# Performance work log

Measured on AMD Instinct MI355X. Metric: run time of the kernel, lower is better.

The kernel has to match this reference:

```python
import jax, jax.numpy as jnp
import numpy as np

N_HEAD = 16
D_MODEL = 1024
D_K = D_MODEL // N_HEAD  # 64, also d_v
B, S = 8, 1024


def setup_inputs() -> dict:
    key = jax.random.key(0)
    ks = jax.random.split(key, 7)
    sc = 1.0 / np.sqrt(D_MODEL)
    return {
        "q": jax.random.normal(ks[0], (B, S, D_MODEL), jnp.float32),
        "k": jax.random.normal(ks[1], (B, S, D_MODEL), jnp.float32),
        "v": jax.random.normal(ks[2], (B, S, D_MODEL), jnp.float32),
        "Wq": jax.random.normal(ks[3], (N_HEAD, D_MODEL, D_K), jnp.float32) * sc,
        "Wk": jax.random.normal(ks[4], (N_HEAD, D_MODEL, D_K), jnp.float32) * sc,
        "Wv": jax.random.normal(ks[5], (D_MODEL, D_K), jnp.float32) * sc,  # shared across heads
        "Wo": jax.random.normal(ks[6], (D_K, D_MODEL), jnp.float32) * (1.0 / np.sqrt(D_K)),
    }


def reference(q, k, v, Wq, Wk, Wv, Wo):
    # Faithful to original: qs, ks, vs are ALL projected from q (k, v args unused),
    # and Wv is shared across all heads. Dropout is identity (rate 0 / eval).
    qs = jnp.einsum('bsd,hdk->hbsk', q, Wq)          # [H,B,S,dk]
    kk = jnp.einsum('bsd,hdk->hbsk', q, Wk)          # [H,B,S,dk]
    vs = jnp.einsum('bsd,dk->bsk', q, Wv)            # [B,S,dv] shared
    scale = 1.0 / jnp.sqrt(jnp.asarray(D_K, jnp.float32))
    scores = jnp.einsum('hbik,hbjk->hbij', qs, kk) * scale  # [H,B,S,S]
    attn = jax.nn.softmax(scores, axis=-1)
    head = jnp.einsum('hbij,bjk->hbik', attn, vs)    # [H,B,S,dv]
    pooled = jnp.mean(head, axis=0)                  # mean over heads, not concat
    out = jnp.einsum('bsk,kd->bsd', pooled, Wo)      # [B,S,d_model]
    return (out, attn)
```

## Files before the change

kernel.cpp:

```cpp
#include <hip/hip_runtime.h>
#include <hip/hip_bf16.h>
#include <stdint.h>

#define NC 2112

typedef __attribute__((ext_vector_type(8))) short bf16x8;
typedef __attribute__((ext_vector_type(4))) float f32x4;

static __device__ __forceinline__ unsigned short f2bf(float f) {
  uint32_t u = __builtin_bit_cast(uint32_t, f);
  u += 0x7FFFu + ((u >> 16) & 1u);
  return (unsigned short)(u >> 16);
}
static __device__ __forceinline__ unsigned short f2bf_n(float f) {
  __hip_bfloat16 h = __float2bfloat16(f);
  return __builtin_bit_cast(unsigned short, h);
}
static __device__ __forceinline__ float bf2f(unsigned short u) {
  return __builtin_bit_cast(float, ((uint32_t)u) << 16);
}
static __device__ __forceinline__ void gload16(const unsigned short* g, unsigned short* l) {
  __builtin_amdgcn_global_load_lds((const __attribute__((address_space(1))) void*)g,
                                   (__attribute__((address_space(3))) void*)l, 16, 0, 0);
}

__global__ void k_convert_q(const float* __restrict__ q, unsigned short* __restrict__ qbf) {
  int i = blockIdx.x * blockDim.x + threadIdx.x;
  float4 v = ((const float4*)q)[i];
  ushort4 o;
  o.x = f2bf(v.x); o.y = f2bf(v.y); o.z = f2bf(v.z); o.w = f2bf(v.w);
  ((ushort4*)qbf)[i] = o;
}

__global__ void k_build_wcatT(const float* __restrict__ Wq, const float* __restrict__ Wk,
                              const float* __restrict__ Wv, unsigned short* __restrict__ wt) {
  int t = blockIdx.x * blockDim.x + threadIdx.x;
  int c = t >> 7;
  int k0 = (t & 127) << 3;
  unsigned short o[8];
#pragma unroll
  for (int i = 0; i < 8; ++i) {
    int k = k0 + i;
    float v;
    if (c < 1024)      v = Wq[((size_t)(c >> 6) * 1024 + k) * 64 + (c & 63)];
    else if (c < 2048) v = Wk[((size_t)((c - 1024) >> 6) * 1024 + k) * 64 + (c & 63)];
    else               v = Wv[(size_t)k * 64 + (c - 2048)];
    o[i] = f2bf(v);
  }
  *(ushort4*)&wt[(size_t)c * 1024 + k0]     = *(ushort4*)&o[0];
  *(ushort4*)&wt[(size_t)c * 1024 + k0 + 4] = *(ushort4*)&o[4];
}

__global__ __launch_bounds__(256) void k_gemm(const unsigned short* __restrict__ A,
                                              const unsigned short* __restrict__ Bt,
                                              unsigned short* __restrict__ C,
                                              unsigned short* __restrict__ vst) {
  __shared__ unsigned short As[128 * 32];
  __shared__ unsigned short Bs[128 * 32];
  const int L = blockIdx.x;
  const int wi = (L & 7) * 136 + (L >> 3);
  const int tn = wi % 17, tm = wi / 17;
  const int rowBase = tm * 128, colBase = tn * 128;
  const int t = threadIdx.x;
  const int wave = t >> 6, lane = t & 63;
  const int wm = wave >> 1, wn = wave & 1;
  const int l15 = lane & 15, l4 = lane >> 4;
  f32x4 acc[4][4] = {};
  for (int kt = 0; kt < 1024; kt += 32) {
#pragma unroll
    for (int i = 0; i < 2; ++i) {
      int e = (t + i * 256) * 8;
      int r = e >> 5, c = e & 31;
      gload16(&A[(size_t)(rowBase + r) * 1024 + kt + c], &As[e]);
      int rb = colBase + r; rb = rb < NC ? rb : (NC - 1);
      gload16(&Bt[(size_t)rb * 1024 + kt + c], &Bs[e]);
    }
    __syncthreads();
    bf16x8 af[4], bfr[4];
#pragma unroll
    for (int m = 0; m < 4; ++m) af[m] = *(const bf16x8*)&As[(wm * 64 + m * 16 + l15) * 32 + l4 * 8];
#pragma unroll
    for (int n = 0; n < 4; ++n) bfr[n] = *(const bf16x8*)&Bs[(wn * 64 + n * 16 + l15) * 32 + l4 * 8];
#pragma unroll
    for (int m = 0; m < 4; ++m)
#pragma unroll
      for (int n = 0; n < 4; ++n)
        acc[m][n] = __builtin_amdgcn_mfma_f32_16x16x32_bf16(af[m], bfr[n], acc[m][n], 0, 0, 0);
    __syncthreads();
  }
#pragma unroll
  for (int m = 0; m < 4; ++m)
#pragma unroll
    for (int n = 0; n < 4; ++n) {
      int col = colBase + wn * 64 + n * 16 + l15;
      int row0 = rowBase + wm * 64 + m * 16 + l4 * 4;
      if (col < 2048) {
#pragma unroll
        for (int i = 0; i < 4; ++i)
          C[(size_t)(row0 + i) * NC + col] = f2bf_n(acc[m][n][i]);
      } else if (col < NC) {
        int d = col - 2048;
#pragma unroll
        for (int i = 0; i < 4; ++i) {
          int rg = row0 + i;
          vst[((size_t)(rg >> 10) * 64 + d) * 1024 + (rg & 1023)] = f2bf_n(acc[m][n][i]);
        }
      }
    }
}

__global__ __launch_bounds__(512, 4) void k_attn(const unsigned short* __restrict__ G,
                                                 const unsigned short* __restrict__ vst,
                                                 float* __restrict__ attn,
                                                 float* __restrict__ head) {
  __shared__ unsigned short SP[32][1032];
  __shared__ float rs[32][8];
  const int L = blockIdx.x;
  const int wi = (L & 7) * 512 + (L >> 3);
  const int qt = wi & 31, b = (wi >> 5) & 7, h = wi >> 8;
  const int t = threadIdx.x, wave = t >> 6, lane = t & 63;
  const int l15 = lane & 15, l4 = lane >> 4;

  const unsigned short* Gb = G + (size_t)b * 1024 * NC;

  bf16x8 qf[2][2];
#pragma unroll
  for (int m = 0; m < 2; ++m)
#pragma unroll
    for (int ks = 0; ks < 2; ++ks)
      qf[m][ks] = *(const bf16x8*)&Gb[(size_t)(qt * 32 + m * 16 + l15) * NC + h * 64 + ks * 32 + l4 * 8];

  const float scale = 0.125f;
  float psum[2][4] = {};
#pragma unroll
  for (int half = 0; half < 2; ++half) {
    bf16x8 kf[4][2];
#pragma unroll
    for (int kt = 0; kt < 4; ++kt) {
      int k0 = wave * 128 + (half * 4 + kt) * 16;
#pragma unroll
      for (int ks = 0; ks < 2; ++ks)
        kf[kt][ks] = *(const bf16x8*)&Gb[(size_t)(k0 + l15) * NC + 1024 + h * 64 + ks * 32 + l4 * 8];
    }
#pragma unroll
    for (int kt = 0; kt < 4; ++kt) {
      int k0 = wave * 128 + (half * 4 + kt) * 16;
      f32x4 s0 = {}, s1 = {};
      __builtin_amdgcn_s_setprio(1);
      s0 = __builtin_amdgcn_mfma_f32_16x16x32_bf16(qf[0][0], kf[kt][0], s0, 0, 0, 0);
      s0 = __builtin_amdgcn_mfma_f32_16x16x32_bf16(qf[0][1], kf[kt][1], s0, 0, 0, 0);
      s1 = __builtin_amdgcn_mfma_f32_16x16x32_bf16(qf[1][0], kf[kt][0], s1, 0, 0, 0);
      s1 = __builtin_amdgcn_mfma_f32_16x16x32_bf16(qf[1][1], kf[kt][1], s1, 0, 0, 0);
      __builtin_amdgcn_s_setprio(0);
#pragma unroll
      for (int i = 0; i < 4; ++i) {
        unsigned short u0 = f2bf_n(__expf(s0[i] * scale));
        unsigned short u1 = f2bf_n(__expf(s1[i] * scale));
        SP[l4 * 4 + i][k0 + l15]      = u0;
        SP[16 + l4 * 4 + i][k0 + l15] = u1;
        psum[0][i] += bf2f(u0);
        psum[1][i] += bf2f(u1);
      }
    }
  }
#pragma unroll
  for (int off = 1; off < 16; off <<= 1)
#pragma unroll
    for (int m = 0; m < 2; ++m)
#pragma unroll
      for (int i = 0; i < 4; ++i)
        psum[m][i] += __shfl_xor(psum[m][i], off);
  if (l15 == 0) {
#pragma unroll
    for (int m = 0; m < 2; ++m)
#pragma unroll
      for (int i = 0; i < 4; ++i)
        rs[m * 16 + l4 * 4 + i][wave] = psum[m][i];
  }
  __syncthreads();

  const int wm = wave >> 2, wn = wave & 3;
  float winv[4], pinv[4];
#pragma unroll
  for (int rr = 0; rr < 4; ++rr) {
    int row = wave * 4 + rr;
    float4 a = *(const float4*)&rs[row][0];
    float4 c = *(const float4*)&rs[row][4];
    winv[rr] = 1.0f / (a.x + a.y + a.z + a.w + c.x + c.y + c.z + c.w);
  }
#pragma unroll
  for (int i = 0; i < 4; ++i) {
    int row = wm * 16 + l4 * 4 + i;
    float4 a = *(const float4*)&rs[row][0];
    float4 c = *(const float4*)&rs[row][4];
    pinv[i] = 1.0f / (a.x + a.y + a.z + a.w + c.x + c.y + c.z + c.w);
  }

  size_t attn_base = ((size_t)(h * 8 + b) * 1024 + (size_t)qt * 32) * 1024;
#pragma unroll
  for (int rr = 0; rr < 4; ++rr) {
    int row = wave * 4 + rr;
    float inv = winv[rr];
#pragma unroll
    for (int c = 0; c < 2; ++c) {
      uint4 u = *(const uint4*)&SP[row][c * 512 + lane * 8];
      f32x4 p0 = {bf2f((unsigned short)(u.x & 0xFFFF)) * inv,
                  bf2f((unsigned short)(u.x >> 16)) * inv,
                  bf2f((unsigned short)(u.y & 0xFFFF)) * inv,
                  bf2f((unsigned short)(u.y >> 16)) * inv};
      f32x4 p1 = {bf2f((unsigned short)(u.z & 0xFFFF)) * inv,
                  bf2f((unsigned short)(u.z >> 16)) * inv,
                  bf2f((unsigned short)(u.w & 0xFFFF)) * inv,
                  bf2f((unsigned short)(u.w >> 16)) * inv};
      float* ab = &attn[attn_base + (size_t)row * 1024 + c * 512 + lane * 8];
      __builtin_nontemporal_store(p0, (f32x4*)ab);
      __builtin_nontemporal_store(p1, (f32x4*)(ab + 4));
    }
  }

  const unsigned short* vb = vst + ((size_t)b * 64 + wn * 16 + l15) * 1024;
  const unsigned short* pr = &SP[wm * 16 + l15][0];
  f32x4 o0 = {}, o1 = {};
  __builtin_amdgcn_s_setprio(1);
#pragma unroll 8
  for (int jt = 0; jt < 32; jt += 2) {
    bf16x8 pa0 = *(const bf16x8*)&pr[jt * 32 + l4 * 8];
    bf16x8 bv0 = *(const bf16x8*)&vb[jt * 32 + l4 * 8];
    o0 = __builtin_amdgcn_mfma_f32_16x16x32_bf16(pa0, bv0, o0, 0, 0, 0);
    bf16x8 pa1 = *(const bf16x8*)&pr[(jt + 1) * 32 + l4 * 8];
    bf16x8 bv1 = *(const bf16x8*)&vb[(jt + 1) * 32 + l4 * 8];
    o1 = __builtin_amdgcn_mfma_f32_16x16x32_bf16(pa1, bv1, o1, 0, 0, 0);
  }
  __builtin_amdgcn_s_setprio(0);
  float* hb = head + (((size_t)(h * 8 + b) * 1024) + qt * 32 + wm * 16) * 64 + wn * 16;
#pragma unroll
  for (int i = 0; i < 4; ++i)
    hb[(size_t)(l4 * 4 + i) * 64 + l15] = (o0[i] + o1[i]) * pinv[i];
}

__global__ __launch_bounds__(256) void k_final(const float* __restrict__ head,
                                               const float* __restrict__ Wo,
                                               float* __restrict__ out) {
  __shared__ float Ps[32][68];
  __shared__ float Ws[64][132];
  const int rt = blockIdx.x;
  const int r0 = rt * 32;
  const int t = threadIdx.x;
#pragma unroll
  for (int j = 0; j < 2; ++j) {
    int e = t + j * 256;
    int r = e >> 4, k4 = (e & 15) * 4;
    float4 acc = {0.f, 0.f, 0.f, 0.f};
#pragma unroll
    for (int hh = 0; hh < 16; ++hh) {
      float4 v = *(const float4*)&head[((size_t)hh * 8192 + r0 + r) * 64 + k4];
      acc.x += v.x; acc.y += v.y; acc.z += v.z; acc.w += v.w;
    }
    const float s = 1.0f / 16.0f;
    Ps[r][k4] = acc.x * s; Ps[r][k4 + 1] = acc.y * s;
    Ps[r][k4 + 2] = acc.z * s; Ps[r][k4 + 3] = acc.w * s;
  }
  const int ty = t >> 4, tx = t & 15;
  for (int dt = 0; dt < 8; ++dt) {
    int d0 = dt * 128;
#pragma unroll
    for (int j = 0; j < 8; ++j) {
      int e = t + j * 256;
      int k = e >> 5, c4 = (e & 31) * 4;
      *(float4*)&Ws[k][c4] = *(const float4*)&Wo[(size_t)k * 1024 + d0 + c4];
    }
    __syncthreads();
    float acc[2][8] = {};
    for (int k = 0; k < 64; ++k) {
      float a0 = Ps[ty * 2][k], a1 = Ps[ty * 2 + 1][k];
      float4 b0 = *(const float4*)&Ws[k][tx * 8];
      float4 b1 = *(const float4*)&Ws[k][tx * 8 + 4];
      acc[0][0] += a0 * b0.x; acc[0][1] += a0 * b0.y; acc[0][2] += a0 * b0.z; acc[0][3] += a0 * b0.w;
      acc[0][4] += a0 * b1.x; acc[0][5] += a0 * b1.y; acc[0][6] += a0 * b1.z; acc[0][7] += a0 * b1.w;
      acc[1][0] += a1 * b0.x; acc[1][1] += a1 * b0.y; acc[1][2] += a1 * b0.z; acc[1][3] += a1 * b0.w;
      acc[1][4] += a1 * b1.x; acc[1][5] += a1 * b1.y; acc[1][6] += a1 * b1.z; acc[1][7] += a1 * b1.w;
    }
#pragma unroll
    for (int i = 0; i < 2; ++i) {
      float4 v0 = {acc[i][0], acc[i][1], acc[i][2], acc[i][3]};
      float4 v1 = {acc[i][4], acc[i][5], acc[i][6], acc[i][7]};
      size_t o = (size_t)(r0 + ty * 2 + i) * 1024 + d0 + tx * 8;
      *(float4*)&out[o]     = v0;
      *(float4*)&out[o + 4] = v1;
    }
    __syncthreads();
  }
}

extern "C" void kernel_launch(void* const* d_in, const int* in_sizes, int n_in,
                              void* d_out, int out_size, void* d_ws, size_t ws_size,
                              hipStream_t stream) {
  const float* q  = (const float*)d_in[0];
  const float* Wq = (const float*)d_in[3];
  const float* Wk = (const float*)d_in[4];
  const float* Wv = (const float*)d_in[5];
  const float* Wo = (const float*)d_in[6];

  char* ws = (char*)d_ws;
  unsigned short* qbf   = (unsigned short*)(ws + 0);
  unsigned short* wcatT = (unsigned short*)(ws + 16777216);
  unsigned short* G     = (unsigned short*)(ws + 21102592);
  unsigned short* vst   = (unsigned short*)(ws + 55705600);
  float*          head  = (float*)(ws + 56754176);

  float* out  = (float*)d_out;
  float* attn = out + (size_t)8 * 1024 * 1024;

  hipLaunchKernelGGL(k_convert_q,   dim3(8192), dim3(256), 0, stream, q, qbf);
  hipLaunchKernelGGL(k_build_wcatT, dim3(1056), dim3(256), 0, stream, Wq, Wk, Wv, wcatT);
  hipLaunchKernelGGL(k_gemm,        dim3(1088), dim3(256), 0, stream, qbf, wcatT, G, vst);
  hipLaunchKernelGGL(k_attn,        dim3(4096), dim3(512), 0, stream, G, vst, attn, head);
  hipLaunchKernelGGL(k_final,       dim3(256),  dim3(256), 0, stream, head, Wo, out);
}
```

Measured before the change: 355.7 us.

## Halve attention query tile to 16 rows and split PV over key halves

The attention kernel now handles 16 query rows per block instead of 32, which doubles the grid and halves shared memory for the probability tile. Launch bounds now request 8 blocks per CU instead of 4, to raise occupancy. The PV product is split across two key halves per wave group and reduced through shared memory with an extra barrier. In exchange, each K tile is reused by fewer query rows, so K loads per output roughly double, and the extra sync adds latency.

```diff
diff --git a/kernel.cpp b/kernel.cpp
--- a/kernel.cpp
+++ b/kernel.cpp
@@ -109,97 +109,86 @@
     }
 }
 
-__global__ __launch_bounds__(512, 4) void k_attn(const unsigned short* __restrict__ G,
+__global__ __launch_bounds__(512, 8) void k_attn(const unsigned short* __restrict__ G,
                                                  const unsigned short* __restrict__ vst,
                                                  float* __restrict__ attn,
                                                  float* __restrict__ head) {
-  __shared__ unsigned short SP[32][1032];
-  __shared__ float rs[32][8];
+  __shared__ unsigned short SP[16][1032];
+  __shared__ float rs[16][8];
+  __shared__ float red[4][16][17];
   const int L = blockIdx.x;
-  const int wi = (L & 7) * 512 + (L >> 3);
-  const int qt = wi & 31, b = (wi >> 5) & 7, h = wi >> 8;
+  const int wi = (L & 7) * 1024 + (L >> 3);
+  const int qt = wi & 63, b = (wi >> 6) & 7, h = wi >> 9;
   const int t = threadIdx.x, wave = t >> 6, lane = t & 63;
   const int l15 = lane & 15, l4 = lane >> 4;
+  const float scale = 0.125f;
 
   const unsigned short* Gb = G + (size_t)b * 1024 * NC;
 
-  bf16x8 qf[2][2];
-#pragma unroll
-  for (int m = 0; m < 2; ++m)
-#pragma unroll
-    for (int ks = 0; ks < 2; ++ks)
-      qf[m][ks] = *(const bf16x8*)&Gb[(size_t)(qt * 32 + m * 16 + l15) * NC + h * 64 + ks * 32 + l4 * 8];
-
-  const float scale = 0.125f;
-  float psum[2][4] = {};
-#pragma unroll
-  for (int half = 0; half < 2; ++half) {
-    bf16x8 kf[4][2];
-#pragma unroll
-    for (int kt = 0; kt < 4; ++kt) {
-      int k0 = wave * 128 + (half * 4 + kt) * 16;
+  bf16x8 qf[2];
+#pragma unroll
+  for (int ks = 0; ks < 2; ++ks)
+    qf[ks] = *(const bf16x8*)&Gb[(size_t)(qt * 16 + l15) * NC + h * 64 + ks * 32 + l4 * 8];
+
+  float psum[4] = {};
+#pragma unroll
+  for (int half = 0; half < 4; ++half) {
+    bf16x8 kf[2][2];
+#pragma unroll
+    for (int kt = 0; kt < 2; ++kt) {
+      int k0 = wave * 128 + (half * 2 + kt) * 16;
 #pragma unroll
       for (int ks = 0; ks < 2; ++ks)
         kf[kt][ks] = *(const bf16x8*)&Gb[(size_t)(k0 + l15) * NC + 1024 + h * 64 + ks * 32 + l4 * 8];
     }
 #pragma unroll
-    for (int kt = 0; kt < 4; ++kt) {
-      int k0 = wave * 128 + (half * 4 + kt) * 16;
-      f32x4 s0 = {}, s1 = {};
+    for (int kt = 0; kt < 2; ++kt) {
+      int k0 = wave * 128 + (half * 2 + kt) * 16;
+      f32x4 s = {};
       __builtin_amdgcn_s_setprio(1);
-      s0 = __builtin_amdgcn_mfma_f32_16x16x32_bf16(qf[0][0], kf[kt][0], s0, 0, 0, 0);
-      s0 = __builtin_amdgcn_mfma_f32_16x16x32_bf16(qf[0][1], kf[kt][1], s0, 0, 0, 0);
-      s1 = __builtin_amdgcn_mfma_f32_16x16x32_bf16(qf[1][0], kf[kt][0], s1, 0, 0, 0);
-      s1 = __builtin_amdgcn_mfma_f32_16x16x32_bf16(qf[1][1], kf[kt][1], s1, 0, 0, 0);
+      s = __builtin_amdgcn_mfma_f32_16x16x32_bf16(qf[0], kf[kt][0], s, 0, 0, 0);
+      s = __builtin_amdgcn_mfma_f32_16x16x32_bf16(qf[1], kf[kt][1], s, 0, 0, 0);
       __builtin_amdgcn_s_setprio(0);
 #pragma unroll
       for (int i = 0; i < 4; ++i) {
-        unsigned short u0 = f2bf_n(__expf(s0[i] * scale));
-        unsigned short u1 = f2bf_n(__expf(s1[i] * scale));
-        SP[l4 * 4 + i][k0 + l15]      = u0;
-        SP[16 + l4 * 4 + i][k0 + l15] = u1;
-        psum[0][i] += bf2f(u0);
-        psum[1][i] += bf2f(u1);
+        unsigned short u = f2bf_n(__expf(s[i] * scale));
+        SP[l4 * 4 + i][k0 + l15] = u;
+        psum[i] += bf2f(u);
       }
     }
   }
 #pragma unroll
   for (int off = 1; off < 16; off <<= 1)
 #pragma unroll
-    for (int m = 0; m < 2; ++m)
-#pragma unroll
-      for (int i = 0; i < 4; ++i)
-        psum[m][i] += __shfl_xor(psum[m][i], off);
+    for (int i = 0; i < 4; ++i)
+      psum[i] += __shfl_xor(psum[i], off);
   if (l15 == 0) {
 #pragma unroll
-    for (int m = 0; m < 2; ++m)
-#pragma unroll
-      for (int i = 0; i < 4; ++i)
-        rs[m * 16 + l4 * 4 + i][wave] = psum[m][i];
+    for (int i = 0; i < 4; ++i)
+      rs[l4 * 4 + i][wave] = psum[i];
   }
   __syncthreads();
 
-  const int wm = wave >> 2, wn = wave & 3;
-  float winv[4], pinv[4];
-#pragma unroll
-  for (int rr = 0; rr < 4; ++rr) {
-    int row = wave * 4 + rr;
+  float winv[2], pinv[4];
+#pragma unroll
+  for (int rr = 0; rr < 2; ++rr) {
+    int row = wave * 2 + rr;
     float4 a = *(const float4*)&rs[row][0];
     float4 c = *(const float4*)&rs[row][4];
     winv[rr] = 1.0f / (a.x + a.y + a.z + a.w + c.x + c.y + c.z + c.w);
   }
 #pragma unroll
   for (int i = 0; i < 4; ++i) {
-    int row = wm * 16 + l4 * 4 + i;
+    int row = l4 * 4 + i;
     float4 a = *(const float4*)&rs[row][0];
     float4 c = *(const float4*)&rs[row][4];
     pinv[i] = 1.0f / (a.x + a.y + a.z + a.w + c.x + c.y + c.z + c.w);
   }
 
-  size_t attn_base = ((size_t)(h * 8 + b) * 1024 + (size_t)qt * 32) * 1024;
-#pragma unroll
-  for (int rr = 0; rr < 4; ++rr) {
-    int row = wave * 4 + rr;
+  size_t attn_base = ((size_t)(h * 8 + b) * 1024 + (size_t)qt * 16) * 1024;
+#pragma unroll
+  for (int rr = 0; rr < 2; ++rr) {
+    int row = wave * 2 + rr;
     float inv = winv[rr];
 #pragma unroll
     for (int c = 0; c < 2; ++c) {
@@ -218,12 +207,13 @@
     }
   }
 
-  const unsigned short* vb = vst + ((size_t)b * 64 + wn * 16 + l15) * 1024;
-  const unsigned short* pr = &SP[wm * 16 + l15][0];
+  const int n = wave & 3, jh = wave >> 2;
+  const unsigned short* vb = vst + ((size_t)b * 64 + n * 16 + l15) * 1024 + jh * 512;
+  const unsigned short* pr = &SP[l15][jh * 512];
   f32x4 o0 = {}, o1 = {};
   __builtin_amdgcn_s_setprio(1);
-#pragma unroll 8
-  for (int jt = 0; jt < 32; jt += 2) {
+#pragma unroll 4
+  for (int jt = 0; jt < 16; jt += 2) {
     bf16x8 pa0 = *(const bf16x8*)&pr[jt * 32 + l4 * 8];
     bf16x8 bv0 = *(const bf16x8*)&vb[jt * 32 + l4 * 8];
     o0 = __builtin_amdgcn_mfma_f32_16x16x32_bf16(pa0, bv0, o0, 0, 0, 0);
@@ -232,10 +222,19 @@
     o1 = __builtin_amdgcn_mfma_f32_16x16x32_bf16(pa1, bv1, o1, 0, 0, 0);
   }
   __builtin_amdgcn_s_setprio(0);
-  float* hb = head + (((size_t)(h * 8 + b) * 1024) + qt * 32 + wm * 16) * 64 + wn * 16;
-#pragma unroll
-  for (int i = 0; i < 4; ++i)
-    hb[(size_t)(l4 * 4 + i) * 64 + l15] = (o0[i] + o1[i]) * pinv[i];
+  if (jh == 1) {
+#pragma unroll
+    for (int i = 0; i < 4; ++i)
+      red[n][l4 * 4 + i][l15] = o0[i] + o1[i];
+  }
+  __syncthreads();
+  if (jh == 0) {
+    float* hb = head + (((size_t)(h * 8 + b) * 1024) + qt * 16) * 64 + n * 16;
+#pragma unroll
+    for (int i = 0; i < 4; ++i)
+      hb[(size_t)(l4 * 4 + i) * 64 + l15] =
+          (o0[i] + o1[i] + red[n][l4 * 4 + i][l15]) * pinv[i];
+  }
 }
 
 __global__ __launch_bounds__(256) void k_final(const float* __restrict__ head,
@@ -314,6 +313,6 @@
   hipLaunchKernelGGL(k_convert_q,   dim3(8192), dim3(256), 0, stream, q, qbf);
   hipLaunchKernelGGL(k_build_wcatT, dim3(1056), dim3(256), 0, stream, Wq, Wk, Wv, wcatT);
   hipLaunchKernelGGL(k_gemm,        dim3(1088), dim3(256), 0, stream, qbf, wcatT, G, vst);
-  hipLaunchKernelGGL(k_attn,        dim3(4096), dim3(512), 0, stream, G, vst, attn, head);
+  hipLaunchKernelGGL(k_attn,        dim3(8192), dim3(512), 0, stream, G, vst, attn, head);
   hipLaunchKernelGGL(k_final,       dim3(256),  dim3(256), 0, stream, head, Wo, out);
 }
```

Result: slower. 398.8 us (+12.1%).
